# Performance work log

Hardware: AMD Instinct MI355X
Metric: run time of the kernel (lower is better)

Reference implementation:

```python
import jax, jax.numpy as jnp
import numpy as np

B, S, R, C = 1, 512, 128, 256  # batch, MSA depth, residues, channels
H, DH = 8, 32                  # heads, per-head dim (H*DH == C here)
EPS = 1e-5


def setup_inputs() -> dict:
    key = jax.random.key(0)
    ks = jax.random.split(key, 8)
    sc = 0.02
    return {
        "x1d": jax.random.normal(ks[0], (B, S, R, C), jnp.float32),
        "ln_w": jnp.ones((C,), jnp.float32),
        "ln_b": jnp.zeros((C,), jnp.float32),
        "wq": jax.random.normal(ks[1], (C, H * DH), jnp.float32) * sc,
        "wk": jax.random.normal(ks[2], (C, H * DH), jnp.float32) * sc,
        "wv": jax.random.normal(ks[3], (C, H * DH), jnp.float32) * sc,
        "wg": jax.random.normal(ks[4], (C, H * DH), jnp.float32) * sc,
        "bg": jnp.zeros((H * DH,), jnp.float32),
        "wf": jax.random.normal(ks[5], (H * DH, C), jnp.float32) * sc,
        "bf": jnp.zeros((C,), jnp.float32),
    }


def reference(x1d, ln_w, ln_b, wq, wk, wv, wg, bg, wf, bf):
    # [B, S, R, C] -> [B, R, S, C]: attend along MSA depth (columns)
    x = jnp.swapaxes(x1d, -2, -3)
    mu = jnp.mean(x, axis=-1, keepdims=True)
    var = jnp.var(x, axis=-1, keepdims=True)
    xn = (x - mu) * jax.lax.rsqrt(var + EPS) * ln_w + ln_b
    shp = xn.shape[:-1] + (H, DH)  # [B, R, S, H, DH]
    gate = jax.nn.sigmoid((xn @ wg + bg).reshape(shp))
    q = (xn @ wq).reshape(shp)
    k = (xn @ wk).reshape(shp)
    v = (xn @ wv).reshape(shp)
    scale = 1.0 / np.sqrt(DH).astype(np.float32)
    # aff: [B, R, H, S, S]
    aff = jnp.einsum('brihc,brjhc->brhij', q * scale, k)
    w = jax.nn.softmax(aff, axis=-1)
    o = jnp.einsum('brhij,brjhc->brihc', w, v) * gate  # [B, R, S, H, DH]
    out = o.reshape(o.shape[:-2] + (H * DH,)) @ wf + bf
    return jnp.swapaxes(out, -2, -3)  # back to [B, S, R, C]
```

## Files before the change

kernel.cpp:

```cpp
#include <hip/hip_runtime.h>

#define S_ 512
#define R_ 128
#define C_ 256
#define H_ 8
#define DH_ 32
#define M_ (R_ * S_)
#define EPS_ 1e-5f

typedef unsigned short u16;
typedef unsigned int u32;
typedef short bf16x8 __attribute__((ext_vector_type(8)));
typedef float f32x4 __attribute__((ext_vector_type(4)));

#define MFMA(a, b, c) __builtin_amdgcn_mfma_f32_16x16x32_bf16(a, b, c, 0, 0, 0)

static __device__ inline u16 f2bf(float f) {
    union { float f; u32 u; } t;
    t.f = f;
    return (u16)((t.u + 0x7FFFu + ((t.u >> 16) & 1u)) >> 16);
}
static __device__ inline float bf2f(u16 v) {
    union { u32 u; float f; } t;
    t.u = ((u32)v) << 16;
    return t.f;
}
static __device__ inline float ex2(float x) {
    float r;
    asm("v_exp_f32 %0, %1" : "=v"(r) : "v"(x));
    return r;
}
static __device__ inline u32 packtrunc(float a, float b) {
    return __builtin_amdgcn_perm(__float_as_uint(b), __float_as_uint(a),
                                 0x07060302u);
}

__global__ __launch_bounds__(256) void lnxn_kernel(const float* __restrict__ x,
                                                   const float* __restrict__ lnw,
                                                   const float* __restrict__ lnb,
                                                   u16* __restrict__ xnb) {
    int wave = threadIdx.x >> 6, lane = threadIdx.x & 63;
    int n = (blockIdx.x << 2) + wave;
    int r = n >> 9, s = n & (S_ - 1);
    const float4 v = ((const float4*)(x + (size_t)(s * R_ + r) * C_))[lane];
    float sum = v.x + v.y + v.z + v.w;
    float sq = v.x * v.x + v.y * v.y + v.z * v.z + v.w * v.w;
#pragma unroll
    for (int off = 32; off; off >>= 1) {
        sum += __shfl_xor(sum, off);
        sq += __shfl_xor(sq, off);
    }
    float mu = sum * (1.0f / C_);
    float rstd = rsqrtf(sq * (1.0f / C_) - mu * mu + EPS_);
    float4 w4 = ((const float4*)lnw)[lane];
    float4 b4 = ((const float4*)lnb)[lane];
    ushort4 st;
    st.x = f2bf((v.x - mu) * rstd * w4.x + b4.x);
    st.y = f2bf((v.y - mu) * rstd * w4.y + b4.y);
    st.z = f2bf((v.z - mu) * rstd * w4.z + b4.z);
    st.w = f2bf((v.w - mu) * rstd * w4.w + b4.w);
    *(ushort4*)(xnb + (size_t)n * C_ + lane * 4) = st;
}

__global__ __launch_bounds__(256) void wcvt_kernel(
    const float* __restrict__ wq, const float* __restrict__ wk,
    const float* __restrict__ wv, const float* __restrict__ wg,
    const float* __restrict__ wf, u16* __restrict__ wcat_t,
    u16* __restrict__ wf_t) {
    __shared__ __align__(16) float tile[32][33];
    const int z = blockIdx.z;
    const float* __restrict__ W =
        (z == 0) ? wq : (z == 1) ? wk : (z == 2) ? wv : (z == 3) ? wg : wf;
    u16* __restrict__ dst = (z < 4) ? (wcat_t + (size_t)z * C_ * C_) : wf_t;
    const int tid = threadIdx.x;
    int rk = tid >> 3, c4 = tid & 7;
    float4 t4 = *(const float4*)&W[(size_t)(blockIdx.x * 32 + rk) * C_ +
                                   blockIdx.y * 32 + c4 * 4];
    tile[rk][c4 * 4 + 0] = t4.x;
    tile[rk][c4 * 4 + 1] = t4.y;
    tile[rk][c4 * 4 + 2] = t4.z;
    tile[rk][c4 * 4 + 3] = t4.w;
    __syncthreads();
    int rn = tid >> 3, k4 = tid & 7;
    ushort4 st;
    st.x = f2bf(tile[k4 * 4 + 0][rn]);
    st.y = f2bf(tile[k4 * 4 + 1][rn]);
    st.z = f2bf(tile[k4 * 4 + 2][rn]);
    st.w = f2bf(tile[k4 * 4 + 3][rn]);
    *(ushort4*)(dst + (size_t)(blockIdx.y * 32 + rn) * C_ + blockIdx.x * 32 +
                k4 * 4) = st;
}

__global__ __launch_bounds__(256) void proj_kernel(
    const u16* __restrict__ xnb, const u16* __restrict__ wcat_t,
    const float* __restrict__ bg, u16* __restrict__ qb, u16* __restrict__ kb,
    u16* __restrict__ vb, u16* __restrict__ gb) {
    __shared__ __align__(16) char smem[128 * 272];
    u16* As = (u16*)smem;
    u16* Bs = (u16*)(smem + 16384);

    const int tid = threadIdx.x;
    const int l = tid & 63, wid = tid >> 6;
    const int g = l >> 4, ql = l & 15;
    const int wm = wid >> 1, wn = wid & 1;
    const int id = blockIdx.x;
    const int xcd = id & 7, j = id >> 3;
    const int ntile = j & 7;
    const int mtile = (j >> 3) * 8 + xcd;
    const int n0 = ntile << 7;
    const int m0 = mtile << 7;
    const int z = ntile >> 1;
    u16* __restrict__ O = (z == 0) ? qb : (z == 1) ? kb : (z == 2) ? vb : gb;

    const f32x4 zz = {0.f, 0.f, 0.f, 0.f};
    f32x4 acc[4][4];
#pragma unroll
    for (int i = 0; i < 4; ++i)
#pragma unroll
        for (int j2 = 0; j2 < 4; ++j2) acc[i][j2] = zz;

    for (int k0 = 0; k0 < C_; k0 += 64) {
        __syncthreads();
#pragma unroll
        for (int rep = 0; rep < 4; ++rep) {
            int idx = tid + rep * 256;
            int row = idx >> 3, c = idx & 7;
            *(uint4*)((char*)As + row * 128 + ((c * 16) ^ ((row & 7) << 4))) =
                *(const uint4*)(xnb + (size_t)(m0 + row) * C_ + k0 + c * 8);
            *(uint4*)((char*)Bs + row * 128 + ((c * 16) ^ ((row & 7) << 4))) =
                *(const uint4*)(wcat_t + (size_t)(n0 + row) * C_ + k0 + c * 8);
        }
        __syncthreads();
#pragma unroll
        for (int ks = 0; ks < 2; ++ks) {
            bf16x8 a[4], b[4];
#pragma unroll
            for (int mf = 0; mf < 4; ++mf) {
                int row = wm * 64 + mf * 16 + ql;
                a[mf] = *(const bf16x8*)((const char*)As + row * 128 +
                                         ((ks * 64 + g * 16) ^ ((row & 7) << 4)));
            }
#pragma unroll
            for (int nf = 0; nf < 4; ++nf) {
                int row = wn * 64 + nf * 16 + ql;
                b[nf] = *(const bf16x8*)((const char*)Bs + row * 128 +
                                         ((ks * 64 + g * 16) ^ ((row & 7) << 4)));
            }
#pragma unroll
            for (int mf = 0; mf < 4; ++mf)
#pragma unroll
                for (int nf = 0; nf < 4; ++nf)
                    acc[mf][nf] = MFMA(a[mf], b[nf], acc[mf][nf]);
        }
    }

    __syncthreads();
    u16* Cs = (u16*)smem;
#pragma unroll
    for (int nf = 0; nf < 4; ++nf) {
        int ncol = wn * 64 + nf * 16 + ql;
        float bgv = (z == 3) ? bg[(n0 + ncol) & 255] : 0.0f;
#pragma unroll
        for (int mf = 0; mf < 4; ++mf) {
            int mrow = wm * 64 + mf * 16 + g * 4;
#pragma unroll
            for (int i = 0; i < 4; ++i) {
                float v = acc[mf][nf][i];
                if (z == 0) v *= 0.25505654003290507f;
                else if (z == 3) v = 1.0f / (1.0f + __expf(-(v + bgv)));
                Cs[(mrow + i) * 136 + ncol] = f2bf(v);
            }
        }
    }
    __syncthreads();
    const int nz0 = (n0 & 255);
#pragma unroll
    for (int rep = 0; rep < 8; ++rep) {
        int idx = tid + rep * 256;
        int row = idx >> 4, c = idx & 15;
        *(uint4*)(O + (size_t)(m0 + row) * C_ + nz0 + c * 8) =
            *(const uint4*)((const char*)Cs + row * 272 + c * 16);
    }
}

__global__ __launch_bounds__(256) void attn_kernel(
    const u16* __restrict__ qb, const u16* __restrict__ kb,
    const u16* __restrict__ vb, const u16* __restrict__ gb,
    u16* __restrict__ ob) {
    __shared__ __align__(16) u16 Klds[64 * 36];
    __shared__ __align__(16) u16 Vt[32 * 76];
    const int id = blockIdx.x;
    const int xcd = id & 7, j = id >> 3;
    const int half = j & 1;
    const int rh = (j >> 1) * 8 + xcd;
    const int r = rh >> 3, h = rh & 7;
    const int tid = threadIdx.x;
    const int l = tid & 63, wid = tid >> 6;
    const int g = l >> 4, ql = l & 15;
    const int mbase = r * S_ + half * 256 + wid * 64;
    const int hoff = h * DH_;
    const f32x4 zz = {0.f, 0.f, 0.f, 0.f};
    const bf16x8 onesf = {(short)0x3F80, (short)0x3F80, (short)0x3F80,
                          (short)0x3F80, (short)0x3F80, (short)0x3F80,
                          (short)0x3F80, (short)0x3F80};

    bf16x8 qf[4];
#pragma unroll
    for (int nf = 0; nf < 4; ++nf)
        qf[nf] = *(const bf16x8*)(qb + (size_t)(mbase + nf * 16 + ql) * C_ +
                                  hoff + g * 8);

    f32x4 o[2][4];
    f32x4 dsacc[4];
#pragma unroll
    for (int j2 = 0; j2 < 4; ++j2) {
        o[0][j2] = zz;
        o[1][j2] = zz;
        dsacc[j2] = zz;
    }

    for (int j0 = 0; j0 < S_; j0 += 64) {
        __syncthreads();
        {
            int row = tid >> 2, c = tid & 3;
            const size_t gsrc = (size_t)(r * S_ + j0 + row) * C_ + hoff + c * 8;
            uint4 kv4 = *(const uint4*)(kb + gsrc);
            *(uint2*)((char*)Klds + row * 72 + c * 16) = make_uint2(kv4.x, kv4.y);
            *(uint2*)((char*)Klds + row * 72 + c * 16 + 8) =
                make_uint2(kv4.z, kv4.w);
            bf16x8 vv = *(const bf16x8*)(vb + gsrc);
#pragma unroll
            for (int jj = 0; jj < 8; ++jj)
                Vt[(c * 8 + jj) * 76 + row] = (u16)vv[jj];
        }
        __syncthreads();
        bf16x8 kf[4];
#pragma unroll
        for (int mf = 0; mf < 4; ++mf) {
            const char* krow = (const char*)Klds + (mf * 16 + ql) * 72 + g * 16;
            union { bf16x8 v; uint2 u2[2]; } ku;
            ku.u2[0] = *(const uint2*)(krow);
            ku.u2[1] = *(const uint2*)(krow + 8);
            kf[mf] = ku.v;
        }
#pragma unroll
        for (int sub = 0; sub < 2; ++sub) {
            f32x4 s0[4], s1[4];
#pragma unroll
            for (int nf = 0; nf < 4; ++nf) {
                s0[nf] = MFMA(kf[sub * 2 + 0], qf[nf], zz);
                s1[nf] = MFMA(kf[sub * 2 + 1], qf[nf], zz);
            }
            bf16x8 vf[2];
#pragma unroll
            for (int mv = 0; mv < 2; ++mv) {
                const char* vrow = (const char*)Vt + (mv * 16 + ql) * 152;
                union { bf16x8 v; uint2 u2[2]; } vu;
                vu.u2[0] = *(const uint2*)(vrow + (sub * 32 + g * 4) * 2);
                vu.u2[1] = *(const uint2*)(vrow + (sub * 32 + 16 + g * 4) * 2);
                vf[mv] = vu.v;
            }
#pragma unroll
            for (int nf = 0; nf < 4; ++nf) {
                union { bf16x8 v; u32 u[4]; } pu;
                pu.u[0] = packtrunc(ex2(s0[nf][0]), ex2(s0[nf][1]));
                pu.u[1] = packtrunc(ex2(s0[nf][2]), ex2(s0[nf][3]));
                pu.u[2] = packtrunc(ex2(s1[nf][0]), ex2(s1[nf][1]));
                pu.u[3] = packtrunc(ex2(s1[nf][2]), ex2(s1[nf][3]));
                dsacc[nf] = MFMA(onesf, pu.v, dsacc[nf]);
                o[0][nf] = MFMA(vf[0], pu.v, o[0][nf]);
                o[1][nf] = MFMA(vf[1], pu.v, o[1][nf]);
            }
        }
    }

#pragma unroll
    for (int nf = 0; nf < 4; ++nf) {
        float inv = 1.0f / dsacc[nf][0];
        size_t rowoff = (size_t)(mbase + nf * 16 + ql) * C_ + hoff;
#pragma unroll
        for (int mv = 0; mv < 2; ++mv) {
            size_t off = rowoff + mv * 16 + g * 4;
            const ushort4 gv = *(const ushort4*)(gb + off);
            ushort4 st;
            st.x = f2bf(o[mv][nf][0] * inv * bf2f(gv.x));
            st.y = f2bf(o[mv][nf][1] * inv * bf2f(gv.y));
            st.z = f2bf(o[mv][nf][2] * inv * bf2f(gv.z));
            st.w = f2bf(o[mv][nf][3] * inv * bf2f(gv.w));
            *(ushort4*)(ob + off) = st;
        }
    }
}

__global__ __launch_bounds__(256) void outproj_kernel(
    const u16* __restrict__ ob, const u16* __restrict__ wf_t,
    const float* __restrict__ bfb, float* __restrict__ out) {
    __shared__ __align__(16) u16 As[128 * 64];
    __shared__ __align__(16) u16 Bs[128 * 64];
    const int tid = threadIdx.x;
    const int l = tid & 63, wid = tid >> 6;
    const int g = l >> 4, ql = l & 15;
    const int wm = wid >> 1, wn = wid & 1;
    const int id = blockIdx.x;
    const int xcd = id & 7, j = id >> 3;
    const int ntile = j & 1;
    const int mtile = (j >> 1) * 8 + xcd;
    const int m0 = mtile << 7;
    const int n0 = ntile << 7;

    const f32x4 zz = {0.f, 0.f, 0.f, 0.f};
    f32x4 acc[4][4];
#pragma unroll
    for (int i = 0; i < 4; ++i)
#pragma unroll
        for (int j2 = 0; j2 < 4; ++j2) acc[i][j2] = zz;

    for (int k0 = 0; k0 < C_; k0 += 64) {
        __syncthreads();
#pragma unroll
        for (int rep = 0; rep < 4; ++rep) {
            int idx = tid + rep * 256;
            int row = idx >> 3, c = idx & 7;
            *(uint4*)((char*)As + row * 128 + ((c * 16) ^ ((row & 7) << 4))) =
                *(const uint4*)(ob + (size_t)(m0 + row) * C_ + k0 + c * 8);
            *(uint4*)((char*)Bs + row * 128 + ((c * 16) ^ ((row & 7) << 4))) =
                *(const uint4*)(wf_t + (size_t)(n0 + row) * C_ + k0 + c * 8);
        }
        __syncthreads();
#pragma unroll
        for (int ks = 0; ks < 2; ++ks) {
            bf16x8 a[4], b[4];
#pragma unroll
            for (int mf = 0; mf < 4; ++mf) {
                int row = wm * 64 + mf * 16 + ql;
                a[mf] = *(const bf16x8*)((const char*)As + row * 128 +
                                         ((ks * 64 + g * 16) ^ ((row & 7) << 4)));
            }
#pragma unroll
            for (int nf = 0; nf < 4; ++nf) {
                int row = wn * 64 + nf * 16 + ql;
                b[nf] = *(const bf16x8*)((const char*)Bs + row * 128 +
                                         ((ks * 64 + g * 16) ^ ((row & 7) << 4)));
            }
#pragma unroll
            for (int mf = 0; mf < 4; ++mf)
#pragma unroll
                for (int nf = 0; nf < 4; ++nf)
                    acc[mf][nf] = MFMA(a[mf], b[nf], acc[mf][nf]);
        }
    }

#pragma unroll
    for (int nf = 0; nf < 4; ++nf) {
        int n_g = n0 + wn * 64 + nf * 16 + ql;
        float bfv = bfb[n_g];
#pragma unroll
        for (int mf = 0; mf < 4; ++mf) {
            int m = m0 + wm * 64 + mf * 16 + g * 4;
#pragma unroll
            for (int i = 0; i < 4; ++i) {
                int mi = m + i;
                int r = mi >> 9, s = mi & (S_ - 1);
                out[(size_t)(s * R_ + r) * C_ + n_g] = acc[mf][nf][i] + bfv;
            }
        }
    }
}

extern "C" void kernel_launch(void* const* d_in, const int* in_sizes, int n_in,
                              void* d_out, int out_size, void* d_ws, size_t ws_size,
                              hipStream_t stream) {
    const float* x = (const float*)d_in[0];
    const float* lnw = (const float*)d_in[1];
    const float* lnb = (const float*)d_in[2];
    const float* wq = (const float*)d_in[3];
    const float* wk = (const float*)d_in[4];
    const float* wv = (const float*)d_in[5];
    const float* wg = (const float*)d_in[6];
    const float* bg = (const float*)d_in[7];
    const float* wf = (const float*)d_in[8];
    const float* bfb = (const float*)d_in[9];
    float* out = (float*)d_out;

    u16* ws = (u16*)d_ws;
    const size_t NC = (size_t)M_ * C_;
    u16* xnb = ws;
    u16* wcat = xnb + NC;
    u16* wft = wcat + 1024 * 256;
    u16* qb = wft + 256 * 256;
    u16* kb = qb + NC;
    u16* vb = kb + NC;
    u16* gb = vb + NC;
    u16* obuf = gb + NC;

    lnxn_kernel<<<M_ / 4, 256, 0, stream>>>(x, lnw, lnb, xnb);
    wcvt_kernel<<<dim3(8, 8, 5), 256, 0, stream>>>(wq, wk, wv, wg, wf, wcat, wft);
    proj_kernel<<<4096, 256, 0, stream>>>(xnb, wcat, bg, qb, kb, vb, gb);
    attn_kernel<<<2048, 256, 0, stream>>>(qb, kb, vb, gb, obuf);
    outproj_kernel<<<1024, 256, 0, stream>>>(obuf, wft, bfb, out);
}
```

Measured before the change: 186.9 us.

## Double-buffer K/V tiles in attention kernel with register prefetch

The attention kernel now uses two LDS buffers for K and transposed V. The next tile's global loads are issued into registers before the current tile's MFMA work and written to the other buffer afterwards, so only one barrier per iteration is needed instead of two. This is meant to hide global load latency behind compute, at the cost of double the LDS footprint and extra live registers.

```diff
diff --git a/kernel.cpp b/kernel.cpp
--- a/kernel.cpp
+++ b/kernel.cpp
@@ -187,8 +187,8 @@
     const u16* __restrict__ qb, const u16* __restrict__ kb,
     const u16* __restrict__ vb, const u16* __restrict__ gb,
     u16* __restrict__ ob) {
-    __shared__ __align__(16) u16 Klds[64 * 36];
-    __shared__ __align__(16) u16 Vt[32 * 76];
+    __shared__ __align__(16) u16 Klds[2][64 * 36];
+    __shared__ __align__(16) u16 Vt[2][32 * 76];
     const int id = blockIdx.x;
     const int xcd = id & 7, j = id >> 3;
     const int half = j & 1;
@@ -204,11 +204,27 @@
                           (short)0x3F80, (short)0x3F80, (short)0x3F80,
                           (short)0x3F80, (short)0x3F80};
 
+    const int srow = tid >> 2, sc = tid & 3;
+    const size_t gbase = (size_t)(r * S_ + srow) * C_ + hoff + sc * 8;
+
     bf16x8 qf[4];
 #pragma unroll
     for (int nf = 0; nf < 4; ++nf)
         qf[nf] = *(const bf16x8*)(qb + (size_t)(mbase + nf * 16 + ql) * C_ +
                                   hoff + g * 8);
+
+    {
+        uint4 k4 = *(const uint4*)(kb + gbase);
+        bf16x8 v8 = *(const bf16x8*)(vb + gbase);
+        *(uint2*)((char*)&Klds[0][0] + srow * 72 + sc * 16) =
+            make_uint2(k4.x, k4.y);
+        *(uint2*)((char*)&Klds[0][0] + srow * 72 + sc * 16 + 8) =
+            make_uint2(k4.z, k4.w);
+#pragma unroll
+        for (int jj = 0; jj < 8; ++jj)
+            Vt[0][(sc * 8 + jj) * 76 + srow] = (u16)v8[jj];
+    }
+    __syncthreads();
 
     f32x4 o[2][4];
     f32x4 dsacc[4];
@@ -219,25 +235,20 @@
         dsacc[j2] = zz;
     }
 
-    for (int j0 = 0; j0 < S_; j0 += 64) {
-        __syncthreads();
-        {
-            int row = tid >> 2, c = tid & 3;
-            const size_t gsrc = (size_t)(r * S_ + j0 + row) * C_ + hoff + c * 8;
-            uint4 kv4 = *(const uint4*)(kb + gsrc);
-            *(uint2*)((char*)Klds + row * 72 + c * 16) = make_uint2(kv4.x, kv4.y);
-            *(uint2*)((char*)Klds + row * 72 + c * 16 + 8) =
-                make_uint2(kv4.z, kv4.w);
-            bf16x8 vv = *(const bf16x8*)(vb + gsrc);
-#pragma unroll
-            for (int jj = 0; jj < 8; ++jj)
-                Vt[(c * 8 + jj) * 76 + row] = (u16)vv[jj];
-        }
-        __syncthreads();
+    for (int t = 0; t < 8; ++t) {
+        const int cur = t & 1;
+        uint4 knext;
+        bf16x8 vnext;
+        if (t < 7) {
+            const size_t gsrc = gbase + (size_t)((t + 1) * 64) * C_;
+            knext = *(const uint4*)(kb + gsrc);
+            vnext = *(const bf16x8*)(vb + gsrc);
+        }
         bf16x8 kf[4];
 #pragma unroll
         for (int mf = 0; mf < 4; ++mf) {
-            const char* krow = (const char*)Klds + (mf * 16 + ql) * 72 + g * 16;
+            const char* krow =
+                (const char*)&Klds[cur][0] + (mf * 16 + ql) * 72 + g * 16;
             union { bf16x8 v; uint2 u2[2]; } ku;
             ku.u2[0] = *(const uint2*)(krow);
             ku.u2[1] = *(const uint2*)(krow + 8);
@@ -254,7 +265,7 @@
             bf16x8 vf[2];
 #pragma unroll
             for (int mv = 0; mv < 2; ++mv) {
-                const char* vrow = (const char*)Vt + (mv * 16 + ql) * 152;
+                const char* vrow = (const char*)&Vt[cur][0] + (mv * 16 + ql) * 152;
                 union { bf16x8 v; uint2 u2[2]; } vu;
                 vu.u2[0] = *(const uint2*)(vrow + (sub * 32 + g * 4) * 2);
                 vu.u2[1] = *(const uint2*)(vrow + (sub * 32 + 16 + g * 4) * 2);
@@ -272,6 +283,18 @@
                 o[1][nf] = MFMA(vf[1], pu.v, o[1][nf]);
             }
         }
+        if (t < 7) {
+            u16* kdst = &Klds[cur ^ 1][0];
+            *(uint2*)((char*)kdst + srow * 72 + sc * 16) =
+                make_uint2(knext.x, knext.y);
+            *(uint2*)((char*)kdst + srow * 72 + sc * 16 + 8) =
+                make_uint2(knext.z, knext.w);
+            u16* vdst = &Vt[cur ^ 1][0];
+#pragma unroll
+            for (int jj = 0; jj < 8; ++jj)
+                vdst[(sc * 8 + jj) * 76 + srow] = (u16)vnext[jj];
+        }
+        __syncthreads();
     }
 
 #pragma unroll
```

New measurement: 197.6 us. 1.06x slower.
